# Kernel optimization log

Hardware: AMD Instinct MI355X
Metric: run time of the kernel (lower is better)

Reference implementation:

```python
import jax, jax.numpy as jnp
import numpy as np

BN_EPS = 1e-5


def _pool_features(labels, fx, fy, n_labels):
    # Mean-pool per-pixel features (fx, fy, xx, yy coord maps) over superpixel labels.
    B, _, w, h = labels.shape
    xx = (jnp.arange(w, dtype=jnp.float32) / (w - 1)) * 2.0 - 1.0   # varies along dim 2
    yy = (jnp.arange(h, dtype=jnp.float32) / (h - 1)) * 2.0 - 1.0   # varies along dim 3
    xx_map = jnp.broadcast_to(xx[:, None], (w, h))
    yy_map = jnp.broadcast_to(yy[None, :], (w, h))
    P = w * h
    feats = jnp.stack([
        fx[:, 0].reshape(B, P),
        fy[:, 0].reshape(B, P),
        jnp.broadcast_to(xx_map.reshape(1, P), (B, P)),
        jnp.broadcast_to(yy_map.reshape(1, P), (B, P)),
    ], axis=-1).reshape(B * P, 4)                                   # [B*P, 4]
    seg = (labels[:, 0].reshape(B, P)
           + n_labels * jnp.arange(B, dtype=jnp.int32)[:, None]).reshape(-1)
    sums = jax.ops.segment_sum(feats, seg, num_segments=B * n_labels)        # [B*K, 4]
    counts = jax.ops.segment_sum(jnp.ones((B * P,), jnp.float32), seg,
                                 num_segments=B * n_labels)                  # [B*K]
    return sums / jnp.maximum(counts, 1.0)[:, None]


def _bn(x, g, b):
    # BatchNorm1d in training mode: batch statistics over the token dim.
    m = x.mean(axis=0)
    v = x.var(axis=0)
    return (x - m) * jax.lax.rsqrt(v + BN_EPS) * g + b


def reference(labels, fx, fy, frame_idx, n_frames, n_labels,
              conv_w, conv_b, bn1_g, bn1_b, lin_w, lin_b, bn2_g, bn2_b):
    pooled = _pool_features(labels, fx, fy, n_labels)               # [B*K, 4] = (fx, fy, xx, yy)
    t = jnp.repeat(frame_idx.astype(jnp.float32) / (n_frames - 1), n_labels)  # [B*K]
    x = jnp.concatenate([t[:, None], pooled], axis=1)               # [B*K, 5]
    x = x @ conv_w.T + conv_b                                       # Conv1d(5,64,1) == linear
    x = jax.nn.relu(_bn(x, bn1_g, bn1_b))
    x = x @ lin_w.T + lin_b                                         # Linear(64,32)
    x = jax.nn.relu(_bn(x, bn2_g, bn2_b))
    nrm = jnp.linalg.norm(x, axis=1, keepdims=True)
    return x / jnp.maximum(nrm, 1e-8)


def setup_inputs() -> dict:
    key = jax.random.key(0)
    ks = jax.random.split(key, 12)
    B, H, W, K = 16, 512, 512, 1024
    labels = jax.random.randint(ks[0], (B, 1, H, W), 0, K, dtype=jnp.int32)
    fx = jax.random.normal(ks[1], (B, 1, H, W), dtype=jnp.float32)
    fy = jax.random.normal(ks[2], (B, 1, H, W), dtype=jnp.float32)
    frame_idx = jax.random.randint(ks[3], (B,), 0, 100, dtype=jnp.int32)
    conv_w = jax.random.normal(ks[4], (64, 5), dtype=jnp.float32) * 0.3
    conv_b = jax.random.normal(ks[5], (64,), dtype=jnp.float32) * 0.05
    bn1_g = 1.0 + 0.05 * jax.random.normal(ks[6], (64,), dtype=jnp.float32)
    bn1_b = 0.05 * jax.random.normal(ks[7], (64,), dtype=jnp.float32)
    lin_w = jax.random.normal(ks[8], (32, 64), dtype=jnp.float32) * 0.1
    lin_b = jax.random.normal(ks[9], (32,), dtype=jnp.float32) * 0.05
    bn2_g = 1.0 + 0.05 * jax.random.normal(ks[10], (32,), dtype=jnp.float32)
    bn2_b = 0.05 * jax.random.normal(ks[11], (32,), dtype=jnp.float32)
    return {"labels": labels, "fx": fx, "fy": fy, "frame_idx": frame_idx,
            "n_frames": 100, "n_labels": K,
            "conv_w": conv_w, "conv_b": conv_b, "bn1_g": bn1_g, "bn1_b": bn1_b,
            "lin_w": lin_w, "lin_b": lin_b, "bn2_g": bn2_g, "bn2_b": bn2_b}
```

## Files before the change

### kernel.cpp

```cpp
#include <hip/hip_runtime.h>
#include <math.h>

#define TPB 256
#define TPBP 1024
#define FSCALE 16384.0f
#define INV_FSCALE (1.0f / 16384.0f)
#define FBIAS (1 << 17)
#define FCLAMP 7.0f


__global__ __launch_bounds__(TPBP)
void pool_kernel(const int* __restrict__ labels,
                 const float* __restrict__ fx,
                 const float* __restrict__ fy,
                 float* __restrict__ partial,
                 int K, int H, int W, int wlog, int chunks) {
    extern __shared__ unsigned long long sh[];
    unsigned long long* geo = sh;
    unsigned long long* fxy = sh + K;
    const int tid = threadIdx.x;

    for (int i = tid; i < K; i += TPBP) { geo[i] = 0ull; fxy[i] = 0ull; }
    __syncthreads();

    const int P = H * W;
    const int b = blockIdx.x / chunks;
    const int chunk = blockIdx.x - b * chunks;
    const int chunkP = P / chunks;
    const size_t base = (size_t)b * P + (size_t)chunk * chunkP;
    const int4*   l4p  = (const int4*)(labels + base);
    const float4* fx4p = (const float4*)(fx + base);
    const float4* fy4p = (const float4*)(fy + base);
    const int nvec = chunkP >> 2;

    for (int v = tid; v < nvec; v += TPBP) {
        int4   l4 = l4p[v];
        float4 f4 = fx4p[v];
        float4 g4 = fy4p[v];
        int p0 = chunk * chunkP + (v << 2);
        int   ls[4] = {l4.x, l4.y, l4.z, l4.w};
        float fs[4] = {f4.x, f4.y, f4.z, f4.w};
        float gs[4] = {g4.x, g4.y, g4.z, g4.w};
        #pragma unroll
        for (int s = 0; s < 4; ++s) {
            int p = p0 + s;
            int i, j;
            if (wlog >= 0) { i = p >> wlog; j = p & (W - 1); }
            else           { i = p / W;     j = p - i * W; }
            unsigned long long gadd = ((unsigned long long)i << 40)
                                    | ((unsigned long long)j << 16) | 1ull;
            int qx = __float2int_rn(fminf(fmaxf(fs[s], -FCLAMP), FCLAMP) * FSCALE) + FBIAS;
            int qy = __float2int_rn(fminf(fmaxf(gs[s], -FCLAMP), FCLAMP) * FSCALE) + FBIAS;
            unsigned long long fadd = ((unsigned long long)(unsigned int)qx << 32)
                                    | (unsigned long long)(unsigned int)qy;
            atomicAdd(&geo[ls[s]], gadd);
            atomicAdd(&fxy[ls[s]], fadd);
        }
    }
    __syncthreads();

    const float sx = 2.f / (float)(H - 1);
    const float sy = 2.f / (float)(W - 1);
    float* outp = partial + (size_t)blockIdx.x * K * 5;
    for (int k = tid; k < K; k += TPBP) {
        unsigned long long g = geo[k];
        unsigned long long ff = fxy[k];
        unsigned int ci = (unsigned int)(g & 0xFFFFull);
        float cnt = (float)ci;
        float sj  = (float)(unsigned int)((g >> 16) & 0xFFFFFFull);
        float si  = (float)(unsigned int)(g >> 40);
        long long cbias = (long long)ci << 17;
        float* p = outp + k * 5;
        p[0] = (float)((long long)(ff >> 32) - cbias) * INV_FSCALE;
        p[1] = (float)((long long)(ff & 0xFFFFFFFFull) - cbias) * INV_FSCALE;
        p[2] = sx * si - cnt;
        p[3] = sy * sj - cnt;
        p[4] = cnt;
    }
}

__global__ __launch_bounds__(TPB)
void k_layer1(const float* __restrict__ partial,
              const int* __restrict__ frame_idx,
              const int* __restrict__ n_frames_p,
              const float* __restrict__ conv_w,
              const float* __restrict__ conv_b,
              float* __restrict__ statA,
              float* __restrict__ h1g,
              int K, int N, int chunks) {
    __shared__ float red[320], feat[320], cw[320], cb[64];

    const int tid = threadIdx.x;
    const int bid = blockIdx.x;

    for (int i = tid; i < 320; i += TPB) cw[i] = conv_w[i];
    if (tid < 64) cb[tid] = conv_b[tid];

    const int t0 = bid * 64;
    const int b  = t0 / K;
    const int k0 = t0 - b * K;

    float acc0 = 0.f, acc1 = 0.f;
    const float* pb = partial + ((size_t)b * chunks * K + k0) * 5;
    for (int ch = 0; ch < chunks; ++ch) {
        const float* pc = pb + (size_t)ch * K * 5;
        acc0 += pc[tid];
        if (tid < 64) acc1 += pc[256 + tid];
    }
    red[tid] = acc0;
    if (tid < 64) red[256 + tid] = acc1;
    __syncthreads();

    const int g  = tid >> 6;
    const int tt = tid & 63;
    const int t  = t0 + tt;
    const bool valid = t < N;
    if (g == 0) {
        const float* r = red + tt * 5;
        float inv = 1.f / fmaxf(r[4], 1.f);
        float invnf = 1.f / (float)(n_frames_p[0] - 1);
        feat[tt * 5 + 0] = valid ? (float)frame_idx[b] * invnf : 0.f;
        feat[tt * 5 + 1] = r[0] * inv;
        feat[tt * 5 + 2] = r[1] * inv;
        feat[tt * 5 + 3] = r[2] * inv;
        feat[tt * 5 + 4] = r[3] * inv;
    }
    __syncthreads();

    const float x0 = feat[tt * 5 + 0], x1 = feat[tt * 5 + 1],
                x2 = feat[tt * 5 + 2], x3 = feat[tt * 5 + 3],
                x4 = feat[tt * 5 + 4];
    float hs[16];
    const int c0 = g * 16;
    #pragma unroll
    for (int j = 0; j < 16; ++j) {
        int c = c0 + j;
        const float* w = cw + c * 5;
        float h = cb[c] + w[0]*x0 + w[1]*x1 + w[2]*x2 + w[3]*x3 + w[4]*x4;
        h1g[(size_t)c * N + t] = h;
        hs[j] = valid ? h : 0.f;
    }
    float mySum = 0.f, mySq = 0.f;
    #pragma unroll
    for (int j = 0; j < 16; ++j) {
        float s = hs[j];
        float q = hs[j] * hs[j];
        #pragma unroll
        for (int m = 1; m < 64; m <<= 1) {
            s += __shfl_xor(s, m, 64);
            q += __shfl_xor(q, m, 64);
        }
        if (tt == j) { mySum = s; mySq = q; }
    }
    if (tt < 16) {
        statA[(size_t)bid * 128 + c0 + tt] = mySum;
        statA[(size_t)bid * 128 + 64 + c0 + tt] = mySq;
    }
}

__global__ __launch_bounds__(TPB)
void k_layer2(const float* __restrict__ statA,
              const float* __restrict__ bn1_g,
              const float* __restrict__ bn1_b,
              const float* __restrict__ lin_w,
              const float* __restrict__ lin_b,
              const float* __restrict__ h1g,
              float* __restrict__ statB,
              float* __restrict__ h2g,
              int N) {
    __shared__ float red[320], w2[2048], lb[32];
    __shared__ float sc1[64], sh1[64];
    __shared__ float h1t[64 * 64];

    const int tid = threadIdx.x;
    const int bid = blockIdx.x;
    const int t0 = bid * 64;

    for (int i = tid; i < 2048; i += TPB) w2[i] = lin_w[i];
    if (tid < 32) lb[tid] = lin_b[tid];

    {
        const int col  = tid & 127;
        const int half = tid >> 7;
        float a = 0.f;
        const float* base = statA + (size_t)half * 128 * 128 + col;
        for (int r = 0; r < 128; ++r)
            a += base[(size_t)r * 128];
        red[tid] = a;
    }

    {
        #pragma unroll
        for (int pass = 0; pass < 4; ++pass) {
            int idx = pass * TPB + tid;
            int c = idx >> 4, q = idx & 15;
            float4 v = *(const float4*)(h1g + (size_t)c * N + t0 + q * 4);
            *(float4*)(&h1t[c * 64 + q * 4]) = v;
        }
    }
    __syncthreads();

    if (tid < 64) {
        float su = red[tid] + red[128 + tid];
        float sq = red[64 + tid] + red[192 + tid];
        float invN = 1.f / (float)N;
        float mean = su * invN;
        float var  = sq * invN - mean * mean;
        float s = bn1_g[tid] * rsqrtf(var + 1e-5f);
        sc1[tid] = s;
        sh1[tid] = bn1_b[tid] - mean * s;
    }
    __syncthreads();

    const int g  = tid >> 6;
    const int tt = tid & 63;
    const int t  = t0 + tt;
    const bool valid = t < N;

    float y[64];
    #pragma unroll
    for (int c = 0; c < 64; ++c)
        y[c] = fmaxf(h1t[c * 64 + tt] * sc1[c] + sh1[c], 0.f);

    float hs[8];
    const int o0 = g * 8;
    #pragma unroll
    for (int j = 0; j < 8; ++j) {
        int o = o0 + j;
        const float* wo = w2 + o * 64;
        float acc = lb[o];
        #pragma unroll
        for (int c = 0; c < 64; ++c) acc += wo[c] * y[c];
        h2g[(size_t)o * N + t] = acc;
        hs[j] = valid ? acc : 0.f;
    }
    float mySum = 0.f, mySq = 0.f;
    #pragma unroll
    for (int j = 0; j < 8; ++j) {
        float s = hs[j];
        float q = hs[j] * hs[j];
        #pragma unroll
        for (int m = 1; m < 64; m <<= 1) {
            s += __shfl_xor(s, m, 64);
            q += __shfl_xor(q, m, 64);
        }
        if (tt == j) { mySum = s; mySq = q; }
    }
    if (tt < 8) {
        statB[(size_t)bid * 64 + o0 + tt] = mySum;
        statB[(size_t)bid * 64 + 32 + o0 + tt] = mySq;
    }
}

__global__ __launch_bounds__(TPB)
void k_final(const float* __restrict__ statB,
             const float* __restrict__ bn2_g,
             const float* __restrict__ bn2_b,
             const float* __restrict__ h2g,
             float* __restrict__ out,
             int N) {
    __shared__ float red[256];
    __shared__ float sc2[32], sh2[32];
    __shared__ float h2t[32 * 68];
    __shared__ float ssqp[4 * 64], linv[64];

    const int tid = threadIdx.x;
    const int bid = blockIdx.x;
    const int t0 = bid * 64;

    {
        const int col = tid & 63;
        const int qr  = tid >> 6;
        float a = 0.f;
        const float* base = statB + (size_t)qr * 64 * 64 + col;
        for (int r = 0; r < 64; ++r)
            a += base[(size_t)r * 64];
        red[tid] = a;
    }

    {
        #pragma unroll
        for (int pass = 0; pass < 2; ++pass) {
            int idx = pass * TPB + tid;
            int o = idx >> 4, q = idx & 15;
            float4 v = *(const float4*)(h2g + (size_t)o * N + t0 + q * 4);
            *(float4*)(&h2t[o * 68 + q * 4]) = v;
        }
    }
    __syncthreads();

    if (tid < 32) {
        float su = red[tid] + red[64 + tid] + red[128 + tid] + red[192 + tid];
        float sq = red[32 + tid] + red[96 + tid] + red[160 + tid] + red[224 + tid];
        float invN = 1.f / (float)N;
        float mean = su * invN;
        float var  = sq * invN - mean * mean;
        float s = bn2_g[tid] * rsqrtf(var + 1e-5f);
        sc2[tid] = s;
        sh2[tid] = bn2_b[tid] - mean * s;
    }
    __syncthreads();

    const int g  = tid >> 6;
    const int tt = tid & 63;
    {
        const int o0 = g * 8;
        float ss = 0.f;
        #pragma unroll
        for (int j = 0; j < 8; ++j) {
            int o = o0 + j;
            float v = fmaxf(h2t[o * 68 + tt] * sc2[o] + sh2[o], 0.f);
            h2t[o * 68 + tt] = v;
            ss += v * v;
        }
        ssqp[g * 64 + tt] = ss;
    }
    __syncthreads();
    if (g == 0) {
        float tot = ssqp[tt] + ssqp[64 + tt] + ssqp[128 + tt] + ssqp[192 + tt];
        linv[tt] = 1.f / fmaxf(sqrtf(tot), 1e-8f);
    }
    __syncthreads();

    const int nq = min(512, (N - t0) * 8);
    float4* o4 = (float4*)(out + (size_t)t0 * 32);
    for (int q = tid; q < nq; q += TPB) {
        int tk = q >> 3;
        int oo = (q & 7) * 4;
        float iv = linv[tk];
        o4[q] = make_float4(h2t[(oo + 0) * 68 + tk] * iv,
                            h2t[(oo + 1) * 68 + tk] * iv,
                            h2t[(oo + 2) * 68 + tk] * iv,
                            h2t[(oo + 3) * 68 + tk] * iv);
    }
}

extern "C" void kernel_launch(void* const* d_in, const int* in_sizes, int n_in,
                              void* d_out, int out_size, void* d_ws, size_t ws_size,
                              hipStream_t stream) {
    const int*   labels     = (const int*)d_in[0];
    const float* fx         = (const float*)d_in[1];
    const float* fy         = (const float*)d_in[2];
    const int*   frame_idx  = (const int*)d_in[3];
    const int*   n_frames_p = (const int*)d_in[4];
    const float* conv_w = (const float*)d_in[6];
    const float* conv_b = (const float*)d_in[7];
    const float* bn1_g  = (const float*)d_in[8];
    const float* bn1_b  = (const float*)d_in[9];
    const float* lin_w  = (const float*)d_in[10];
    const float* lin_b  = (const float*)d_in[11];
    const float* bn2_g  = (const float*)d_in[12];
    const float* bn2_b  = (const float*)d_in[13];
    float* out = (float*)d_out;

    const int B = in_sizes[3];
    const int P = in_sizes[0] / B;
    const int W = (int)(sqrt((double)P) + 0.5);
    const int H = P / W;
    const int K = out_size / (B * 32);
    const int N = B * K;

    int wlog = -1;
    if ((W & (W - 1)) == 0) { wlog = 0; while ((1 << wlog) < W) ++wlog; }

    const int nblk = (N + 63) / 64;

    int chunks = 16;
    while (chunks > 1 && (P % (chunks * 4)) != 0) chunks >>= 1;
    while (P / chunks > 16384) chunks <<= 1;

    float* statA   = (float*)d_ws;
    float* statB   = statA + (size_t)nblk * 128;
    float* partial = statB + (size_t)nblk * 64;
    float* h1g     = partial + (size_t)B * chunks * K * 5;
    float* h2g     = h1g + (size_t)64 * N;

    pool_kernel<<<B * chunks, TPBP, (size_t)K * 16, stream>>>(
        labels, fx, fy, partial, K, H, W, wlog, chunks);
    k_layer1<<<nblk, TPB, 0, stream>>>(
        partial, frame_idx, n_frames_p, conv_w, conv_b, statA, h1g, K, N, chunks);
    k_layer2<<<nblk, TPB, 0, stream>>>(
        statA, bn1_g, bn1_b, lin_w, lin_b, h1g, statB, h2g, N);
    k_final<<<nblk, TPB, 0, stream>>>(
        statB, bn2_g, bn2_b, h2g, out, N);
}
```

Baseline: 133.1 us.

## Recompute hidden layers from stored features instead of materializing activations

Instead of writing the 64-channel and 32-channel hidden activations to global memory between kernels, only the 5 pooled input features are stored. The later kernels recompute the conv layer, and the final kernel also recomputes the linear layer from them. The pooled partial output layout is also changed to structure-of-arrays so writes and reads coalesce. This trades extra FMA work and per-block weight loads to shared memory for much less global-memory traffic on the MLP stages. Stat reductions now use gridDim-based row counts rather than hard-coded 128/64.

```diff
diff --git a/kernel.cpp b/kernel.cpp
--- a/kernel.cpp
+++ b/kernel.cpp
@@ -70,25 +70,25 @@
         float sj  = (float)(unsigned int)((g >> 16) & 0xFFFFFFull);
         float si  = (float)(unsigned int)(g >> 40);
         long long cbias = (long long)ci << 17;
-        float* p = outp + k * 5;
-        p[0] = (float)((long long)(ff >> 32) - cbias) * INV_FSCALE;
-        p[1] = (float)((long long)(ff & 0xFFFFFFFFull) - cbias) * INV_FSCALE;
-        p[2] = sx * si - cnt;
-        p[3] = sy * sj - cnt;
-        p[4] = cnt;
+        outp[0 * K + k] = (float)((long long)(ff >> 32) - cbias) * INV_FSCALE;
+        outp[1 * K + k] = (float)((long long)(ff & 0xFFFFFFFFull) - cbias) * INV_FSCALE;
+        outp[2 * K + k] = sx * si - cnt;
+        outp[3 * K + k] = sy * sj - cnt;
+        outp[4 * K + k] = cnt;
     }
 }
 
 __global__ __launch_bounds__(TPB)
-void k_layer1(const float* __restrict__ partial,
-              const int* __restrict__ frame_idx,
-              const int* __restrict__ n_frames_p,
-              const float* __restrict__ conv_w,
-              const float* __restrict__ conv_b,
-              float* __restrict__ statA,
-              float* __restrict__ h1g,
-              int K, int N, int chunks) {
-    __shared__ float red[320], feat[320], cw[320], cb[64];
+void k_feat(const float* __restrict__ partial,
+            const int* __restrict__ frame_idx,
+            const int* __restrict__ n_frames_p,
+            const float* __restrict__ conv_w,
+            const float* __restrict__ conv_b,
+            float* __restrict__ statA,
+            float* __restrict__ featg,
+            int K, int N, int chunks) {
+    __shared__ float red[320];
+    __shared__ float cw[320], cb[64];
 
     const int tid = threadIdx.x;
     const int bid = blockIdx.x;
@@ -100,36 +100,40 @@
     const int b  = t0 / K;
     const int k0 = t0 - b * K;
 
-    float acc0 = 0.f, acc1 = 0.f;
-    const float* pb = partial + ((size_t)b * chunks * K + k0) * 5;
+    const int f1 = tid >> 6, kk = tid & 63;
+    float a0 = 0.f, a1 = 0.f;
+    const float* pb = partial + (size_t)b * chunks * K * 5;
     for (int ch = 0; ch < chunks; ++ch) {
         const float* pc = pb + (size_t)ch * K * 5;
-        acc0 += pc[tid];
-        if (tid < 64) acc1 += pc[256 + tid];
-    }
-    red[tid] = acc0;
-    if (tid < 64) red[256 + tid] = acc1;
+        a0 += pc[(size_t)f1 * K + k0 + kk];
+        if (tid < 64) a1 += pc[(size_t)4 * K + k0 + tid];
+    }
+    red[f1 * 64 + kk] = a0;
+    if (tid < 64) red[4 * 64 + tid] = a1;
     __syncthreads();
 
     const int g  = tid >> 6;
     const int tt = tid & 63;
     const int t  = t0 + tt;
     const bool valid = t < N;
-    if (g == 0) {
-        const float* r = red + tt * 5;
-        float inv = 1.f / fmaxf(r[4], 1.f);
-        float invnf = 1.f / (float)(n_frames_p[0] - 1);
-        feat[tt * 5 + 0] = valid ? (float)frame_idx[b] * invnf : 0.f;
-        feat[tt * 5 + 1] = r[0] * inv;
-        feat[tt * 5 + 2] = r[1] * inv;
-        feat[tt * 5 + 3] = r[2] * inv;
-        feat[tt * 5 + 4] = r[3] * inv;
-    }
-    __syncthreads();
-
-    const float x0 = feat[tt * 5 + 0], x1 = feat[tt * 5 + 1],
-                x2 = feat[tt * 5 + 2], x3 = feat[tt * 5 + 3],
-                x4 = feat[tt * 5 + 4];
+
+    const float cntv = red[4 * 64 + tt];
+    const float inv  = 1.f / fmaxf(cntv, 1.f);
+    const float invnf = 1.f / (float)(n_frames_p[0] - 1);
+    const float x0 = valid ? (float)frame_idx[b] * invnf : 0.f;
+    const float x1 = red[0 * 64 + tt] * inv;
+    const float x2 = red[1 * 64 + tt] * inv;
+    const float x3 = red[2 * 64 + tt] * inv;
+    const float x4 = red[3 * 64 + tt] * inv;
+
+    if (g == 0 && valid) {
+        featg[(size_t)0 * N + t] = x0;
+        featg[(size_t)1 * N + t] = x1;
+        featg[(size_t)2 * N + t] = x2;
+        featg[(size_t)3 * N + t] = x3;
+        featg[(size_t)4 * N + t] = x4;
+    }
+
     float hs[16];
     const int c0 = g * 16;
     #pragma unroll
@@ -137,7 +141,6 @@
         int c = c0 + j;
         const float* w = cw + c * 5;
         float h = cb[c] + w[0]*x0 + w[1]*x1 + w[2]*x2 + w[3]*x3 + w[4]*x4;
-        h1g[(size_t)c * N + t] = h;
         hs[j] = valid ? h : 0.f;
     }
     float mySum = 0.f, mySq = 0.f;
@@ -159,23 +162,29 @@
 }
 
 __global__ __launch_bounds__(TPB)
-void k_layer2(const float* __restrict__ statA,
-              const float* __restrict__ bn1_g,
-              const float* __restrict__ bn1_b,
-              const float* __restrict__ lin_w,
-              const float* __restrict__ lin_b,
-              const float* __restrict__ h1g,
-              float* __restrict__ statB,
-              float* __restrict__ h2g,
-              int N) {
-    __shared__ float red[320], w2[2048], lb[32];
+void k_stat2(const float* __restrict__ statA,
+             const float* __restrict__ bn1_g,
+             const float* __restrict__ bn1_b,
+             const float* __restrict__ conv_w,
+             const float* __restrict__ conv_b,
+             const float* __restrict__ lin_w,
+             const float* __restrict__ lin_b,
+             const float* __restrict__ featg,
+             float* __restrict__ sc1g,
+             float* __restrict__ sh1g,
+             float* __restrict__ statB,
+             int N) {
+    __shared__ float red[256];
+    __shared__ float cw[320], cb[64], w2[2048], lb[32];
     __shared__ float sc1[64], sh1[64];
-    __shared__ float h1t[64 * 64];
 
     const int tid = threadIdx.x;
     const int bid = blockIdx.x;
+    const int nblk = gridDim.x;
     const int t0 = bid * 64;
 
+    for (int i = tid; i < 320; i += TPB) cw[i] = conv_w[i];
+    if (tid < 64) cb[tid] = conv_b[tid];
     for (int i = tid; i < 2048; i += TPB) w2[i] = lin_w[i];
     if (tid < 32) lb[tid] = lin_b[tid];
 
@@ -183,21 +192,22 @@
         const int col  = tid & 127;
         const int half = tid >> 7;
         float a = 0.f;
-        const float* base = statA + (size_t)half * 128 * 128 + col;
-        for (int r = 0; r < 128; ++r)
+        const float* base = statA + (size_t)half * (nblk / 2) * 128 + col;
+        for (int r = 0; r < nblk / 2; ++r)
             a += base[(size_t)r * 128];
         red[tid] = a;
     }
 
-    {
-        #pragma unroll
-        for (int pass = 0; pass < 4; ++pass) {
-            int idx = pass * TPB + tid;
-            int c = idx >> 4, q = idx & 15;
-            float4 v = *(const float4*)(h1g + (size_t)c * N + t0 + q * 4);
-            *(float4*)(&h1t[c * 64 + q * 4]) = v;
-        }
-    }
+    const int g  = tid >> 6;
+    const int tt = tid & 63;
+    const int t  = t0 + tt;
+    const bool valid = t < N;
+
+    const float x0 = featg[(size_t)0 * N + t];
+    const float x1 = featg[(size_t)1 * N + t];
+    const float x2 = featg[(size_t)2 * N + t];
+    const float x3 = featg[(size_t)3 * N + t];
+    const float x4 = featg[(size_t)4 * N + t];
     __syncthreads();
 
     if (tid < 64) {
@@ -209,18 +219,17 @@
         float s = bn1_g[tid] * rsqrtf(var + 1e-5f);
         sc1[tid] = s;
         sh1[tid] = bn1_b[tid] - mean * s;
-    }
-    __syncthreads();
-
-    const int g  = tid >> 6;
-    const int tt = tid & 63;
-    const int t  = t0 + tt;
-    const bool valid = t < N;
+        if (bid == 0) { sc1g[tid] = s; sh1g[tid] = bn1_b[tid] - mean * s; }
+    }
+    __syncthreads();
 
     float y[64];
     #pragma unroll
-    for (int c = 0; c < 64; ++c)
-        y[c] = fmaxf(h1t[c * 64 + tt] * sc1[c] + sh1[c], 0.f);
+    for (int c = 0; c < 64; ++c) {
+        const float* w = cw + c * 5;
+        float h = cb[c] + w[0]*x0 + w[1]*x1 + w[2]*x2 + w[3]*x3 + w[4]*x4;
+        y[c] = fmaxf(h * sc1[c] + sh1[c], 0.f);
+    }
 
     float hs[8];
     const int o0 = g * 8;
@@ -231,7 +240,6 @@
         float acc = lb[o];
         #pragma unroll
         for (int c = 0; c < 64; ++c) acc += wo[c] * y[c];
-        h2g[(size_t)o * N + t] = acc;
         hs[j] = valid ? acc : 0.f;
     }
     float mySum = 0.f, mySq = 0.f;
@@ -253,40 +261,55 @@
 }
 
 __global__ __launch_bounds__(TPB)
-void k_final(const float* __restrict__ statB,
-             const float* __restrict__ bn2_g,
-             const float* __restrict__ bn2_b,
-             const float* __restrict__ h2g,
-             float* __restrict__ out,
-             int N) {
+void k_out(const float* __restrict__ statB,
+           const float* __restrict__ bn2_g,
+           const float* __restrict__ bn2_b,
+           const float* __restrict__ conv_w,
+           const float* __restrict__ conv_b,
+           const float* __restrict__ lin_w,
+           const float* __restrict__ lin_b,
+           const float* __restrict__ featg,
+           const float* __restrict__ sc1g,
+           const float* __restrict__ sh1g,
+           float* __restrict__ out,
+           int N) {
     __shared__ float red[256];
-    __shared__ float sc2[32], sh2[32];
+    __shared__ float cw[320], cb[64], w2[2048], lb[32];
+    __shared__ float sc1[64], sh1[64], sc2[32], sh2[32];
     __shared__ float h2t[32 * 68];
     __shared__ float ssqp[4 * 64], linv[64];
 
     const int tid = threadIdx.x;
     const int bid = blockIdx.x;
+    const int nblk = gridDim.x;
     const int t0 = bid * 64;
+
+    for (int i = tid; i < 320; i += TPB) cw[i] = conv_w[i];
+    if (tid < 64) cb[tid] = conv_b[tid];
+    for (int i = tid; i < 2048; i += TPB) w2[i] = lin_w[i];
+    if (tid < 32) lb[tid] = lin_b[tid];
+    if (tid < 64) { sc1[tid] = sc1g[tid]; sh1[tid] = sh1g[tid]; }
 
     {
         const int col = tid & 63;
         const int qr  = tid >> 6;
         float a = 0.f;
-        const float* base = statB + (size_t)qr * 64 * 64 + col;
-        for (int r = 0; r < 64; ++r)
+        const float* base = statB + (size_t)qr * (nblk / 4) * 64 + col;
+        for (int r = 0; r < nblk / 4; ++r)
             a += base[(size_t)r * 64];
         red[tid] = a;
     }
 
-    {
-        #pragma unroll
-        for (int pass = 0; pass < 2; ++pass) {
-            int idx = pass * TPB + tid;
-            int o = idx >> 4, q = idx & 15;
-            float4 v = *(const float4*)(h2g + (size_t)o * N + t0 + q * 4);
-            *(float4*)(&h2t[o * 68 + q * 4]) = v;
-        }
-    }
+    const int g  = tid >> 6;
+    const int tt = tid & 63;
+    const int t  = t0 + tt;
+    const bool valid = t < N;
+
+    const float x0 = featg[(size_t)0 * N + t];
+    const float x1 = featg[(size_t)1 * N + t];
+    const float x2 = featg[(size_t)2 * N + t];
+    const float x3 = featg[(size_t)3 * N + t];
+    const float x4 = featg[(size_t)4 * N + t];
     __syncthreads();
 
     if (tid < 32) {
@@ -301,15 +324,25 @@
     }
     __syncthreads();
 
-    const int g  = tid >> 6;
-    const int tt = tid & 63;
+    float y[64];
+    #pragma unroll
+    for (int c = 0; c < 64; ++c) {
+        const float* w = cw + c * 5;
+        float h = cb[c] + w[0]*x0 + w[1]*x1 + w[2]*x2 + w[3]*x3 + w[4]*x4;
+        y[c] = fmaxf(h * sc1[c] + sh1[c], 0.f);
+    }
+
     {
         const int o0 = g * 8;
         float ss = 0.f;
         #pragma unroll
         for (int j = 0; j < 8; ++j) {
             int o = o0 + j;
-            float v = fmaxf(h2t[o * 68 + tt] * sc2[o] + sh2[o], 0.f);
+            const float* wo = w2 + o * 64;
+            float acc = lb[o];
+            #pragma unroll
+            for (int c = 0; c < 64; ++c) acc += wo[c] * y[c];
+            float v = fmaxf(acc * sc2[o] + sh2[o], 0.f);
             h2t[o * 68 + tt] = v;
             ss += v * v;
         }
@@ -371,16 +404,19 @@
 
     float* statA   = (float*)d_ws;
     float* statB   = statA + (size_t)nblk * 128;
-    float* partial = statB + (size_t)nblk * 64;
-    float* h1g     = partial + (size_t)B * chunks * K * 5;
-    float* h2g     = h1g + (size_t)64 * N;
+    float* sc1g    = statB + (size_t)nblk * 64;
+    float* sh1g    = sc1g + 64;
+    float* partial = sh1g + 64;
+    float* featg   = partial + (size_t)B * chunks * K * 5;
 
     pool_kernel<<<B * chunks, TPBP, (size_t)K * 16, stream>>>(
         labels, fx, fy, partial, K, H, W, wlog, chunks);
-    k_layer1<<<nblk, TPB, 0, stream>>>(
-        partial, frame_idx, n_frames_p, conv_w, conv_b, statA, h1g, K, N, chunks);
-    k_layer2<<<nblk, TPB, 0, stream>>>(
-        statA, bn1_g, bn1_b, lin_w, lin_b, h1g, statB, h2g, N);
-    k_final<<<nblk, TPB, 0, stream>>>(
-        statB, bn2_g, bn2_b, h2g, out, N);
+    k_feat<<<nblk, TPB, 0, stream>>>(
+        partial, frame_idx, n_frames_p, conv_w, conv_b, statA, featg, K, N, chunks);
+    k_stat2<<<nblk, TPB, 0, stream>>>(
+        statA, bn1_g, bn1_b, conv_w, conv_b, lin_w, lin_b, featg,
+        sc1g, sh1g, statB, N);
+    k_out<<<nblk, TPB, 0, stream>>>(
+        statB, bn2_g, bn2_b, conv_w, conv_b, lin_w, lin_b, featg,
+        sc1g, sh1g, out, N);
 }
```

Result: slower. 188.1 us (+41.3%).

## Use SoA partial layout, shared-memory BN stat reductions, unrolled cross-block sums

Applied to the files above, without the earlier changes.

The pool kernel now writes its per-chunk partial sums feature-major (structure of arrays), so layer1 reads them coalesced per feature. In layer1 and layer2 the per-channel sum and sum-of-squares shuffle reductions are replaced by a transposed shared-memory tile with a two-stage reduction. The cross-block stat reductions in layer2 and the final kernel use a fully unrolled fixed-row path and derive the row count from gridDim rather than hardcoding it. The aim is to cut the shuffle count and the load latency, at the cost of extra shared memory and barriers.

```diff
diff --git a/kernel.cpp b/kernel.cpp
--- a/kernel.cpp
+++ b/kernel.cpp
@@ -70,13 +70,26 @@
         float sj  = (float)(unsigned int)((g >> 16) & 0xFFFFFFull);
         float si  = (float)(unsigned int)(g >> 40);
         long long cbias = (long long)ci << 17;
-        float* p = outp + k * 5;
-        p[0] = (float)((long long)(ff >> 32) - cbias) * INV_FSCALE;
-        p[1] = (float)((long long)(ff & 0xFFFFFFFFull) - cbias) * INV_FSCALE;
-        p[2] = sx * si - cnt;
-        p[3] = sy * sj - cnt;
-        p[4] = cnt;
-    }
+        outp[0 * K + k] = (float)((long long)(ff >> 32) - cbias) * INV_FSCALE;
+        outp[1 * K + k] = (float)((long long)(ff & 0xFFFFFFFFull) - cbias) * INV_FSCALE;
+        outp[2 * K + k] = sx * si - cnt;
+        outp[3 * K + k] = sy * sj - cnt;
+        outp[4 * K + k] = cnt;
+    }
+}
+
+template <int ROWS>
+__device__ __forceinline__ float red_fixed(const float* __restrict__ base, int stride) {
+    float a = 0.f;
+    #pragma unroll
+    for (int r = 0; r < ROWS; ++r) a += base[(size_t)r * stride];
+    return a;
+}
+__device__ __forceinline__ float red_dyn(const float* __restrict__ base, int rows, int stride) {
+    float a = 0.f;
+    #pragma unroll 8
+    for (int r = 0; r < rows; ++r) a += base[(size_t)r * stride];
+    return a;
 }
 
 __global__ __launch_bounds__(TPB)
@@ -88,7 +101,10 @@
               float* __restrict__ statA,
               float* __restrict__ h1g,
               int K, int N, int chunks) {
-    __shared__ float red[320], feat[320], cw[320], cb[64];
+    __shared__ float red[320];
+    __shared__ float cw[320], cb[64];
+    __shared__ float h1t[64 * 65];
+    __shared__ float ps[256], pq[256];
 
     const int tid = threadIdx.x;
     const int bid = blockIdx.x;
@@ -100,37 +116,42 @@
     const int b  = t0 / K;
     const int k0 = t0 - b * K;
 
-    float acc0 = 0.f, acc1 = 0.f;
-    const float* pb = partial + ((size_t)b * chunks * K + k0) * 5;
-    for (int ch = 0; ch < chunks; ++ch) {
-        const float* pc = pb + (size_t)ch * K * 5;
-        acc0 += pc[tid];
-        if (tid < 64) acc1 += pc[256 + tid];
-    }
-    red[tid] = acc0;
-    if (tid < 64) red[256 + tid] = acc1;
+    const int f1 = tid >> 6, kk = tid & 63;
+    float a0 = 0.f, a1 = 0.f;
+    const float* pb = partial + (size_t)b * chunks * K * 5;
+    if (chunks == 16) {
+        #pragma unroll
+        for (int ch = 0; ch < 16; ++ch) {
+            const float* pc = pb + (size_t)ch * K * 5;
+            a0 += pc[(size_t)f1 * K + k0 + kk];
+            if (tid < 64) a1 += pc[(size_t)4 * K + k0 + tid];
+        }
+    } else {
+        #pragma unroll 4
+        for (int ch = 0; ch < chunks; ++ch) {
+            const float* pc = pb + (size_t)ch * K * 5;
+            a0 += pc[(size_t)f1 * K + k0 + kk];
+            if (tid < 64) a1 += pc[(size_t)4 * K + k0 + tid];
+        }
+    }
+    red[f1 * 64 + kk] = a0;
+    if (tid < 64) red[4 * 64 + tid] = a1;
     __syncthreads();
 
     const int g  = tid >> 6;
     const int tt = tid & 63;
     const int t  = t0 + tt;
     const bool valid = t < N;
-    if (g == 0) {
-        const float* r = red + tt * 5;
-        float inv = 1.f / fmaxf(r[4], 1.f);
-        float invnf = 1.f / (float)(n_frames_p[0] - 1);
-        feat[tt * 5 + 0] = valid ? (float)frame_idx[b] * invnf : 0.f;
-        feat[tt * 5 + 1] = r[0] * inv;
-        feat[tt * 5 + 2] = r[1] * inv;
-        feat[tt * 5 + 3] = r[2] * inv;
-        feat[tt * 5 + 4] = r[3] * inv;
-    }
-    __syncthreads();
-
-    const float x0 = feat[tt * 5 + 0], x1 = feat[tt * 5 + 1],
-                x2 = feat[tt * 5 + 2], x3 = feat[tt * 5 + 3],
-                x4 = feat[tt * 5 + 4];
-    float hs[16];
+
+    const float cntv = red[4 * 64 + tt];
+    const float inv  = 1.f / fmaxf(cntv, 1.f);
+    const float invnf = 1.f / (float)(n_frames_p[0] - 1);
+    const float x0 = valid ? (float)frame_idx[b] * invnf : 0.f;
+    const float x1 = red[0 * 64 + tt] * inv;
+    const float x2 = red[1 * 64 + tt] * inv;
+    const float x3 = red[2 * 64 + tt] * inv;
+    const float x4 = red[3 * 64 + tt] * inv;
+
     const int c0 = g * 16;
     #pragma unroll
     for (int j = 0; j < 16; ++j) {
@@ -138,23 +159,27 @@
         const float* w = cw + c * 5;
         float h = cb[c] + w[0]*x0 + w[1]*x1 + w[2]*x2 + w[3]*x3 + w[4]*x4;
         h1g[(size_t)c * N + t] = h;
-        hs[j] = valid ? h : 0.f;
-    }
-    float mySum = 0.f, mySq = 0.f;
-    #pragma unroll
-    for (int j = 0; j < 16; ++j) {
-        float s = hs[j];
-        float q = hs[j] * hs[j];
-        #pragma unroll
-        for (int m = 1; m < 64; m <<= 1) {
-            s += __shfl_xor(s, m, 64);
-            q += __shfl_xor(q, m, 64);
-        }
-        if (tt == j) { mySum = s; mySq = q; }
-    }
-    if (tt < 16) {
-        statA[(size_t)bid * 128 + c0 + tt] = mySum;
-        statA[(size_t)bid * 128 + 64 + c0 + tt] = mySq;
+        h1t[c * 65 + tt] = valid ? h : 0.f;
+    }
+    __syncthreads();
+
+    {
+        const int cc = tid & 63, rr = tid >> 6;
+        float s = 0.f, q = 0.f;
+        #pragma unroll
+        for (int i = 0; i < 16; ++i) {
+            float v = h1t[cc * 65 + rr * 16 + i];
+            s += v; q += v * v;
+        }
+        ps[rr * 64 + cc] = s;
+        pq[rr * 64 + cc] = q;
+    }
+    __syncthreads();
+    if (tid < 64) {
+        float su = ps[tid] + ps[64 + tid] + ps[128 + tid] + ps[192 + tid];
+        float sq = pq[tid] + pq[64 + tid] + pq[128 + tid] + pq[192 + tid];
+        statA[(size_t)bid * 128 + tid] = su;
+        statA[(size_t)bid * 128 + 64 + tid] = sq;
     }
 }
 
@@ -168,12 +193,15 @@
               float* __restrict__ statB,
               float* __restrict__ h2g,
               int N) {
-    __shared__ float red[320], w2[2048], lb[32];
+    __shared__ float red[256], w2[2048], lb[32];
     __shared__ float sc1[64], sh1[64];
     __shared__ float h1t[64 * 64];
+    __shared__ float h2t[32 * 65];
+    __shared__ float ps[256], pq[256];
 
     const int tid = threadIdx.x;
     const int bid = blockIdx.x;
+    const int nblk = gridDim.x;
     const int t0 = bid * 64;
 
     for (int i = tid; i < 2048; i += TPB) w2[i] = lin_w[i];
@@ -182,11 +210,10 @@
     {
         const int col  = tid & 127;
         const int half = tid >> 7;
-        float a = 0.f;
-        const float* base = statA + (size_t)half * 128 * 128 + col;
-        for (int r = 0; r < 128; ++r)
-            a += base[(size_t)r * 128];
-        red[tid] = a;
+        const int rows = nblk >> 1;
+        const float* base = statA + (size_t)half * rows * 128 + col;
+        red[tid] = (rows == 128) ? red_fixed<128>(base, 128)
+                                 : red_dyn(base, rows, 128);
     }
 
     {
@@ -222,7 +249,6 @@
     for (int c = 0; c < 64; ++c)
         y[c] = fmaxf(h1t[c * 64 + tt] * sc1[c] + sh1[c], 0.f);
 
-    float hs[8];
     const int o0 = g * 8;
     #pragma unroll
     for (int j = 0; j < 8; ++j) {
@@ -232,23 +258,28 @@
         #pragma unroll
         for (int c = 0; c < 64; ++c) acc += wo[c] * y[c];
         h2g[(size_t)o * N + t] = acc;
-        hs[j] = valid ? acc : 0.f;
-    }
-    float mySum = 0.f, mySq = 0.f;
-    #pragma unroll
-    for (int j = 0; j < 8; ++j) {
-        float s = hs[j];
-        float q = hs[j] * hs[j];
-        #pragma unroll
-        for (int m = 1; m < 64; m <<= 1) {
-            s += __shfl_xor(s, m, 64);
-            q += __shfl_xor(q, m, 64);
-        }
-        if (tt == j) { mySum = s; mySq = q; }
-    }
-    if (tt < 8) {
-        statB[(size_t)bid * 64 + o0 + tt] = mySum;
-        statB[(size_t)bid * 64 + 32 + o0 + tt] = mySq;
+        h2t[o * 65 + tt] = valid ? acc : 0.f;
+    }
+    __syncthreads();
+
+    {
+        const int o = tid & 31, rr = tid >> 5;
+        float s = 0.f, q = 0.f;
+        #pragma unroll
+        for (int i = 0; i < 8; ++i) {
+            float v = h2t[o * 65 + rr * 8 + i];
+            s += v; q += v * v;
+        }
+        ps[rr * 32 + o] = s;
+        pq[rr * 32 + o] = q;
+    }
+    __syncthreads();
+    if (tid < 32) {
+        float su = 0.f, sq = 0.f;
+        #pragma unroll
+        for (int rr = 0; rr < 8; ++rr) { su += ps[rr * 32 + tid]; sq += pq[rr * 32 + tid]; }
+        statB[(size_t)bid * 64 + tid] = su;
+        statB[(size_t)bid * 64 + 32 + tid] = sq;
     }
 }
 
@@ -266,16 +297,16 @@
 
     const int tid = threadIdx.x;
     const int bid = blockIdx.x;
+    const int nblk = gridDim.x;
     const int t0 = bid * 64;
 
     {
         const int col = tid & 63;
         const int qr  = tid >> 6;
-        float a = 0.f;
-        const float* base = statB + (size_t)qr * 64 * 64 + col;
-        for (int r = 0; r < 64; ++r)
-            a += base[(size_t)r * 64];
-        red[tid] = a;
+        const int rows = nblk >> 2;
+        const float* base = statB + (size_t)qr * rows * 64 + col;
+        red[tid] = (rows == 64) ? red_fixed<64>(base, 64)
+                                : red_dyn(base, rows, 64);
     }
 
     {
```

Result: faster. 127.9 us, median of 2 (-3.9%).
